# Performance work log

Hardware: AMD Instinct MI355X
Metric: run time of the kernel (lower is better)

The kernel has to match this reference:

```python
import jax, jax.numpy as jnp
import numpy as np

PATCH = 8      # patch_size
NFREQ = 8      # fourie_freq


def _fourier_feats(nH, nW, F, dtype):
    # Per-patch positional Fourier features: sin/cos of normalized patch-center
    # coords at F dyadic frequencies for both axes -> [nH, nW, 4F].
    iy = (jnp.arange(nH, dtype=jnp.float32) + 0.5) / nH
    ix = (jnp.arange(nW, dtype=jnp.float32) + 0.5) / nW
    freqs = (2.0 ** jnp.arange(F, dtype=jnp.float32)) * jnp.pi
    fy = iy[:, None] * freqs[None, :]  # [nH, F]
    fx = ix[:, None] * freqs[None, :]  # [nW, F]
    feats = jnp.concatenate([
        jnp.broadcast_to(jnp.sin(fy)[:, None, :], (nH, nW, F)),
        jnp.broadcast_to(jnp.cos(fy)[:, None, :], (nH, nW, F)),
        jnp.broadcast_to(jnp.sin(fx)[None, :, :], (nH, nW, F)),
        jnp.broadcast_to(jnp.cos(fx)[None, :, :], (nH, nW, F)),
    ], axis=-1)
    return feats.astype(dtype)


def setup_inputs() -> dict:
    key = jax.random.key(0)
    ks = jax.random.split(key, 5)
    B, C, H, W = 16, 64, 128, 128
    E, OC, P, F = 8, 64, PATCH, NFREQ
    GC = C + 4 * F  # gate_channel = 96
    x = jax.random.normal(ks[0], (B, C, H, W), jnp.float32)
    expert_w = jax.random.normal(ks[1], (E, OC, C, 3, 3), jnp.float32) * 0.05
    expert_b = jax.random.normal(ks[2], (E, OC), jnp.float32) * 0.05
    gate_w = jax.random.normal(ks[3], (E, GC * P * P), jnp.float32) * 0.02
    gate_b = jnp.zeros((E,), jnp.float32)
    return {"x": x, "expert_w": expert_w, "expert_b": expert_b,
            "gate_w": gate_w, "gate_b": gate_b}


def reference(x, expert_w, expert_b, gate_w, gate_b):
    B, C, H, W = x.shape
    E, OC = expert_w.shape[0], expert_w.shape[1]
    P, F = PATCH, NFREQ
    nH, nW = H // P, W // P

    # --- gating: per-patch softmax over experts ---
    # patches: [B, nH, nW, C, P, P] (matches nn.Flatten over (C,P,P))
    patches = x.reshape(B, C, nH, P, nW, P).transpose(0, 2, 4, 1, 3, 5)
    feats = _fourier_feats(nH, nW, F, x.dtype)                       # [nH,nW,4F]
    pos = jnp.broadcast_to(feats[None, :, :, :, None, None],
                           (B, nH, nW, 4 * F, P, P))
    gate_in = jnp.concatenate([patches, pos], axis=3).reshape(B, nH, nW, -1)
    logits = jnp.einsum('bhwf,ef->bhwe', gate_in, gate_w) + gate_b
    gate = jax.nn.softmax(logits, axis=-1)                           # [B,nH,nW,E]

    # --- experts: all E convs fused into a single conv, then gated combine ---
    wk = expert_w.reshape(E * OC, C, 3, 3)
    y = jax.lax.conv_general_dilated(
        x, wk, window_strides=(1, 1), padding='SAME',
        dimension_numbers=('NCHW', 'OIHW', 'NCHW'))
    y = y + expert_b.reshape(E * OC)[None, :, None, None]
    y = jax.nn.relu(y).reshape(B, E, OC, H, W)

    # upsample per-patch gates to pixel resolution: [B,E,H,W]
    g = gate.transpose(0, 3, 1, 2)                                   # [B,E,nH,nW]
    g = jnp.repeat(jnp.repeat(g, P, axis=2), P, axis=3)
    out = jnp.einsum('behw,bechw->bchw', g, y)                       # [B,OC,H,W]
    return out
```

## Files before the change

kernel.cpp:

```cpp
#include <hip/hip_runtime.h>

typedef short v8s __attribute__((ext_vector_type(8)));
typedef float v4f __attribute__((ext_vector_type(4)));

#define NCH    64
#define NHH    128
#define NWW    128
#define NOC    64
#define KSTEPS 18

#define CSTR 72
#define COLS 66
#define SLAB_BYTES (6 * COLS * CSTR * 2)
#define BBUF_OFF   SLAB_BYTES
#define LDSG_OFF   (SLAB_BYTES + 16384)
#define SMEM_BYTES 73728

__device__ __forceinline__ unsigned short f2bf(float f) {
  unsigned int u = __float_as_uint(f);
  u += 0x7FFFu + ((u >> 16) & 1u);
  return (unsigned short)(u >> 16);
}

__global__ void pack_b_kernel(const float* __restrict__ ew,
                              unsigned short* __restrict__ bp) {
  int f = blockIdx.x * 256 + threadIdx.x;
  int j = f & 7;
  int t = f >> 3;
  int lane = t & 63;
  t >>= 6;
  int nt = t & 3;
  t >>= 2;
  int s = t % KSTEPS;
  int e = t / KSTEPS;
  int k = s * 32 + (lane >> 4) * 8 + j;
  int n = nt * 16 + (lane & 15);
  int khw = k >> 6;
  int c = k & 63;
  bp[f] = f2bf(ew[((e * NOC + n) * NCH + c) * 9 + khw]);
}

__global__ void gate_kernel(const float* __restrict__ x,
                            const float* __restrict__ gw,
                            const float* __restrict__ gb,
                            float* __restrict__ gate_out) {
  int pid = blockIdx.x;
  int pw = pid & 15;
  int ph = (pid >> 4) & 15;
  int b  = pid >> 8;
  int tid = threadIdx.x;

  float cy = (ph + 0.5f) / 16.0f;
  float cx = (pw + 0.5f) / 16.0f;

  float acc[8];
#pragma unroll
  for (int e = 0; e < 8; ++e) acc[e] = 0.f;

  for (int u = tid; u < 1024; u += 256) {
    int ch = u >> 4;
    int pix = (u & 15) * 4;
    int py = pix >> 3;
    int px = pix & 7;
    const float4 xv = *(const float4*)&x[((b * NCH + ch) * NHH + ph * 8 + py) * NWW + pw * 8 + px];
    int fidx = ch * 64 + pix;
#pragma unroll
    for (int e = 0; e < 8; ++e) {
      const float4 wv = *(const float4*)&gw[e * 6144 + fidx];
      acc[e] += xv.x * wv.x + xv.y * wv.y + xv.z * wv.z + xv.w * wv.w;
    }
  }
  for (int u = tid; u < 512; u += 256) {
    int j = u >> 4;
    int g4 = (u & 15) * 4;
    float freq = (float)(1 << (j & 7)) * 3.14159265358979323846f;
    float base = (j < 16) ? cy : cx;
    float a = base * freq;
    float v = ((j >> 3) & 1) ? cosf(a) : sinf(a);
    int fidx = 4096 + j * 64 + g4;
#pragma unroll
    for (int e = 0; e < 8; ++e) {
      const float4 wv = *(const float4*)&gw[e * 6144 + fidx];
      acc[e] += v * (wv.x + wv.y + wv.z + wv.w);
    }
  }

#pragma unroll
  for (int e = 0; e < 8; ++e)
    for (int off = 32; off > 0; off >>= 1)
      acc[e] += __shfl_down(acc[e], off, 64);

  __shared__ float red[8][4];
  int wid = tid >> 6;
  int lane = tid & 63;
  if (lane == 0) {
#pragma unroll
    for (int e = 0; e < 8; ++e) red[e][wid] = acc[e];
  }
  __syncthreads();
  if (tid == 0) {
    float lg[8];
    float mx = -1e30f;
#pragma unroll
    for (int e = 0; e < 8; ++e) {
      lg[e] = red[e][0] + red[e][1] + red[e][2] + red[e][3] + gb[e];
      mx = fmaxf(mx, lg[e]);
    }
    float sum = 0.f;
#pragma unroll
    for (int e = 0; e < 8; ++e) { lg[e] = expf(lg[e] - mx); sum += lg[e]; }
    float inv = 1.0f / sum;
#pragma unroll
    for (int e = 0; e < 8; ++e) gate_out[pid * 8 + e] = lg[e] * inv;
  }
}

__device__ __forceinline__ void load_stage(const unsigned short* __restrict__ bp,
                                           char* smem, int gs, int buf,
                                           int wid, int lane) {
  const char* gsrc = (const char*)bp + gs * 8192 + wid * 2048 + lane * 16;
  char* ldst = smem + BBUF_OFF + buf * 8192 + wid * 2048;
  __builtin_amdgcn_global_load_lds(
      (const __attribute__((address_space(1))) void*)gsrc,
      (__attribute__((address_space(3))) void*)ldst, 16, 0, 0);
  __builtin_amdgcn_global_load_lds(
      (const __attribute__((address_space(1))) void*)(gsrc + 1024),
      (__attribute__((address_space(3))) void*)(ldst + 1024), 16, 0, 0);
}

__global__ __launch_bounds__(256, 2) void moe_conv_kernel(
    const float* __restrict__ x,
    const float* __restrict__ eb,
    const unsigned short* __restrict__ bp,
    const float* __restrict__ gate,
    float* __restrict__ out) {
  __shared__ __align__(16) char smem[SMEM_BYTES];
  unsigned short* slab = (unsigned short*)smem;
  unsigned short* bbufs = (unsigned short*)(smem + BBUF_OFF);
  float* ldsg = (float*)(smem + LDSG_OFF);

  const int tid = threadIdx.x;
  const int bid = blockIdx.x;
  const int wseg = bid & 1;
  const int hq = (bid >> 1) & 31;
  const int b = bid >> 6;
  const int w0 = wseg * 64;
  const int wid = tid >> 6;
  const int lane = tid & 63;
  const int quad = lane >> 4;
  const int l15 = lane & 15;
  const int rp  = wid >> 1;
  const int och = wid & 1;
  const int ntb = och * 2;

  load_stage(bp, smem, 0, 0, wid, lane);

  if (tid < 64) {
    ldsg[tid] = gate[((b * 16 + (hq >> 1)) * 16 + wseg * 8 + (tid >> 3)) * 8 + (tid & 7)];
  }

  const int hbase = hq * 4 - 1;
  const int wbase = w0 - 1;
  for (int flat = tid; flat < 6 * 32 * COLS; flat += 256) {
    int col = flat % COLS;
    int t = flat / COLS;
    int cp = t & 31;
    int r = t >> 5;
    int gh = hbase + r;
    int gw_ = wbase + col;
    float v0 = 0.f, v1 = 0.f;
    if (((unsigned)gh < 128u) && ((unsigned)gw_ < 128u)) {
      const float* px = x + (((b * NCH + cp * 2) * NHH + gh) * NWW + gw_);
      v0 = px[0];
      v1 = px[NHH * NWW];
    }
    unsigned int pk = (unsigned int)f2bf(v0) | ((unsigned int)f2bf(v1) << 16);
    *(unsigned int*)&slab[(r * COLS + col) * CSTR + cp * 2] = pk;
  }
  __syncthreads();

  const v4f vzero = {0.f, 0.f, 0.f, 0.f};
  v4f oacc[8][2];
#pragma unroll
  for (int mt = 0; mt < 8; ++mt) {
    oacc[mt][0] = vzero;
    oacc[mt][1] = vzero;
  }

  const unsigned short* abase = &slab[(rp * 2 * COLS + l15) * CSTR + quad * 8];

  for (int e = 0; e < 8; ++e) {
    v4f vacc[8][2];
#pragma unroll
    for (int mt = 0; mt < 8; ++mt) {
      vacc[mt][0] = vzero;
      vacc[mt][1] = vzero;
    }

#pragma unroll
    for (int st = 0; st < 9; ++st) {
      const int gs = e * 9 + st;
      if (gs > 0) __syncthreads();
      if (gs + 1 < 72) load_stage(bp, smem, gs + 1, (gs + 1) & 1, wid, lane);

      const unsigned short* bstage = bbufs + (gs & 1) * 4096;
#pragma unroll
      for (int sub = 0; sub < 2; ++sub) {
        const int sl = st * 2 + sub;
        const int kh = sl / 6;
        const int kw = (sl / 2) % 3;
        const int ch = sl & 1;
        const v8s b0 = *(const v8s*)(bstage + (sub * 4 + ntb) * 512 + lane * 8);
        const v8s b1 = *(const v8s*)(bstage + (sub * 4 + ntb + 1) * 512 + lane * 8);
#pragma unroll
        for (int mt = 0; mt < 8; ++mt) {
          const v8s a = *(const v8s*)(abase +
              (((mt >> 2) + kh) * COLS + (mt & 3) * 16 + kw) * CSTR + ch * 32);
          vacc[mt][0] = __builtin_amdgcn_mfma_f32_16x16x32_bf16(a, b0, vacc[mt][0], 0, 0, 0);
          vacc[mt][1] = __builtin_amdgcn_mfma_f32_16x16x32_bf16(a, b1, vacc[mt][1], 0, 0, 0);
        }
      }
    }

    float bias0 = eb[e * NOC + ntb * 16 + l15];
    float bias1 = eb[e * NOC + (ntb + 1) * 16 + l15];
#pragma unroll
    for (int mt = 0; mt < 8; ++mt) {
      float g = ldsg[((mt & 3) * 2 + (quad >> 1)) * 8 + e];
#pragma unroll
      for (int r = 0; r < 4; ++r) {
        float v0 = fmaxf(vacc[mt][0][r] + bias0, 0.f);
        float v1 = fmaxf(vacc[mt][1][r] + bias1, 0.f);
        oacc[mt][0][r] += v0 * g;
        oacc[mt][1][r] += v1 * g;
      }
    }
  }

  __syncthreads();
  float* tb = (float*)smem + wid * 4352;
#pragma unroll
  for (int i = 0; i < 2; ++i)
#pragma unroll
    for (int mt = 0; mt < 8; ++mt)
      *(v4f*)(tb + (mt >> 2) * 2176 + (i * 16 + l15) * 68 + (mt & 3) * 16 + quad * 4) =
          oacc[mt][i];

  const int h0 = hq * 4 + rp * 2;
#pragma unroll
  for (int r2 = 0; r2 < 2; ++r2) {
    const int h = h0 + r2;
#pragma unroll
    for (int g4 = 0; g4 < 8; ++g4) {
      const int ocl = g4 * 4 + quad;
      const v4f vv = *(const v4f*)(tb + r2 * 2176 + ocl * 68 + l15 * 4);
      float* dst = out + ((b * NOC + och * 32 + ocl) * NHH + h) * NWW + w0 + l15 * 4;
      *(v4f*)dst = vv;
    }
  }
}

extern "C" void kernel_launch(void* const* d_in, const int* in_sizes, int n_in,
                              void* d_out, int out_size, void* d_ws, size_t ws_size,
                              hipStream_t stream) {
  const float* x  = (const float*)d_in[0];
  const float* ew = (const float*)d_in[1];
  const float* eb = (const float*)d_in[2];
  const float* gw = (const float*)d_in[3];
  const float* gb = (const float*)d_in[4];
  float* out = (float*)d_out;

  unsigned short* bp = (unsigned short*)d_ws;
  float* gate = (float*)((char*)d_ws + 589824);

  hipLaunchKernelGGL(pack_b_kernel, dim3(1152), dim3(256), 0, stream, ew, bp);
  hipLaunchKernelGGL(gate_kernel, dim3(4096), dim3(256), 0, stream, x, gw, gb, gate);
  hipLaunchKernelGGL(moe_conv_kernel, dim3(1024), dim3(256), 0, stream, x, eb, bp, gate, out);
}
```

Baseline: 303.6 us.

## Process expert pairs per stage to reuse A fragments across two experts

Repacks the expert weight buffer so each 8 KB stage holds one k-step for two experts instead of two k-steps for one expert. Each stage's A fragments are then loaded once from LDS and used for both experts' MFMAs, halving A-fragment LDS reads. In exchange, accumulator registers double (two sets of 64 floats of vacc plus oacc), which risks spilling or lower occupancy under launch_bounds(256,2).

```diff
diff --git a/kernel.cpp b/kernel.cpp
--- a/kernel.cpp
+++ b/kernel.cpp
@@ -31,13 +31,14 @@
   t >>= 6;
   int nt = t & 3;
   t >>= 2;
+  int e2 = t & 1;
+  t >>= 1;
   int s = t % KSTEPS;
-  int e = t / KSTEPS;
+  int ep = t / KSTEPS;
+  int e = ep * 2 + e2;
   int k = s * 32 + (lane >> 4) * 8 + j;
   int n = nt * 16 + (lane & 15);
-  int khw = k >> 6;
-  int c = k & 63;
-  bp[f] = f2bf(ew[((e * NOC + n) * NCH + c) * 9 + khw]);
+  bp[f] = f2bf(ew[((e * NOC + n) * NCH + (k & 63)) * 9 + (k >> 6)]);
 }
 
 __global__ void gate_kernel(const float* __restrict__ x,
@@ -189,50 +190,60 @@
 
   const unsigned short* abase = &slab[(rp * 2 * COLS + l15) * CSTR + quad * 8];
 
-  for (int e = 0; e < 8; ++e) {
-    v4f vacc[8][2];
-#pragma unroll
-    for (int mt = 0; mt < 8; ++mt) {
-      vacc[mt][0] = vzero;
-      vacc[mt][1] = vzero;
-    }
-
-#pragma unroll
-    for (int st = 0; st < 9; ++st) {
-      const int gs = e * 9 + st;
+  for (int ep = 0; ep < 4; ++ep) {
+    v4f vacc[2][8][2];
+#pragma unroll
+    for (int e2 = 0; e2 < 2; ++e2)
+#pragma unroll
+      for (int mt = 0; mt < 8; ++mt) {
+        vacc[e2][mt][0] = vzero;
+        vacc[e2][mt][1] = vzero;
+      }
+
+#pragma unroll
+    for (int s = 0; s < KSTEPS; ++s) {
+      const int gs = ep * KSTEPS + s;
       if (gs > 0) __syncthreads();
       if (gs + 1 < 72) load_stage(bp, smem, gs + 1, (gs + 1) & 1, wid, lane);
 
       const unsigned short* bstage = bbufs + (gs & 1) * 4096;
-#pragma unroll
-      for (int sub = 0; sub < 2; ++sub) {
-        const int sl = st * 2 + sub;
-        const int kh = sl / 6;
-        const int kw = (sl / 2) % 3;
-        const int ch = sl & 1;
-        const v8s b0 = *(const v8s*)(bstage + (sub * 4 + ntb) * 512 + lane * 8);
-        const v8s b1 = *(const v8s*)(bstage + (sub * 4 + ntb + 1) * 512 + lane * 8);
+      const int kh = s / 6;
+      const int kw = (s / 2) % 3;
+      const int ch = s & 1;
+
+      v8s af[8];
+#pragma unroll
+      for (int mt = 0; mt < 8; ++mt)
+        af[mt] = *(const v8s*)(abase +
+            (((mt >> 2) + kh) * COLS + (mt & 3) * 16 + kw) * CSTR + ch * 32);
+
+#pragma unroll
+      for (int e2 = 0; e2 < 2; ++e2) {
+        const v8s b0 = *(const v8s*)(bstage + (e2 * 4 + ntb) * 512 + lane * 8);
+        const v8s b1 = *(const v8s*)(bstage + (e2 * 4 + ntb + 1) * 512 + lane * 8);
 #pragma unroll
         for (int mt = 0; mt < 8; ++mt) {
-          const v8s a = *(const v8s*)(abase +
-              (((mt >> 2) + kh) * COLS + (mt & 3) * 16 + kw) * CSTR + ch * 32);
-          vacc[mt][0] = __builtin_amdgcn_mfma_f32_16x16x32_bf16(a, b0, vacc[mt][0], 0, 0, 0);
-          vacc[mt][1] = __builtin_amdgcn_mfma_f32_16x16x32_bf16(a, b1, vacc[mt][1], 0, 0, 0);
+          vacc[e2][mt][0] = __builtin_amdgcn_mfma_f32_16x16x32_bf16(af[mt], b0, vacc[e2][mt][0], 0, 0, 0);
+          vacc[e2][mt][1] = __builtin_amdgcn_mfma_f32_16x16x32_bf16(af[mt], b1, vacc[e2][mt][1], 0, 0, 0);
         }
       }
     }
 
-    float bias0 = eb[e * NOC + ntb * 16 + l15];
-    float bias1 = eb[e * NOC + (ntb + 1) * 16 + l15];
-#pragma unroll
-    for (int mt = 0; mt < 8; ++mt) {
-      float g = ldsg[((mt & 3) * 2 + (quad >> 1)) * 8 + e];
-#pragma unroll
-      for (int r = 0; r < 4; ++r) {
-        float v0 = fmaxf(vacc[mt][0][r] + bias0, 0.f);
-        float v1 = fmaxf(vacc[mt][1][r] + bias1, 0.f);
-        oacc[mt][0][r] += v0 * g;
-        oacc[mt][1][r] += v1 * g;
+#pragma unroll
+    for (int e2 = 0; e2 < 2; ++e2) {
+      const int e = ep * 2 + e2;
+      float bias0 = eb[e * NOC + ntb * 16 + l15];
+      float bias1 = eb[e * NOC + (ntb + 1) * 16 + l15];
+#pragma unroll
+      for (int mt = 0; mt < 8; ++mt) {
+        float g = ldsg[((mt & 3) * 2 + (quad >> 1)) * 8 + e];
+#pragma unroll
+        for (int r = 0; r < 4; ++r) {
+          float v0 = fmaxf(vacc[e2][mt][0][r] + bias0, 0.f);
+          float v1 = fmaxf(vacc[e2][mt][1][r] + bias1, 0.f);
+          oacc[mt][0][r] += v0 * g;
+          oacc[mt][1][r] += v1 * g;
+        }
       }
     }
   }
```

Result: slower. 309.8 us (+2.0%).

## Replace block-wide B double-buffer with per-wave 3-slot DMA ring

Applied to the files above, without the earlier changes.

Each wave now streams only the weight fragments it needs into a private 3-deep LDS ring, using vmcnt waits instead of a block-wide __syncthreads at every K step. The packed weight layout is reordered so each output-channel half is contiguous per step. Gate values move from LDS into a register that is read with shuffles. This removes 72 barriers per block and lets waves drift independently. The cost is redundant weight loads across the two waves sharing an output half, and correctness now depends on hand-written waitcnt counts.

```diff
diff --git a/kernel.cpp b/kernel.cpp
--- a/kernel.cpp
+++ b/kernel.cpp
@@ -12,9 +12,10 @@
 #define CSTR 72
 #define COLS 66
 #define SLAB_BYTES (6 * COLS * CSTR * 2)
-#define BBUF_OFF   SLAB_BYTES
-#define LDSG_OFF   (SLAB_BYTES + 16384)
-#define SMEM_BYTES 73728
+#define RING_OFF   SLAB_BYTES
+#define RING_SLOTS 3
+#define RING_WAVE_BYTES (RING_SLOTS * 2048)
+#define SMEM_BYTES (SLAB_BYTES + 4 * RING_WAVE_BYTES)
 
 __device__ __forceinline__ unsigned short f2bf(float f) {
   unsigned int u = __float_as_uint(f);
@@ -26,18 +27,16 @@
                               unsigned short* __restrict__ bp) {
   int f = blockIdx.x * 256 + threadIdx.x;
   int j = f & 7;
-  int t = f >> 3;
-  int lane = t & 63;
-  t >>= 6;
-  int nt = t & 3;
-  t >>= 2;
+  int lane = (f >> 3) & 63;
+  int i = (f >> 9) & 1;
+  int och = (f >> 10) & 1;
+  int t = f >> 11;
   int s = t % KSTEPS;
   int e = t / KSTEPS;
+  int nt = och * 2 + i;
   int k = s * 32 + (lane >> 4) * 8 + j;
   int n = nt * 16 + (lane & 15);
-  int khw = k >> 6;
-  int c = k & 63;
-  bp[f] = f2bf(ew[((e * NOC + n) * NCH + c) * 9 + khw]);
+  bp[f] = f2bf(ew[((e * NOC + n) * NCH + (k & 63)) * 9 + (k >> 6)]);
 }
 
 __global__ void gate_kernel(const float* __restrict__ x,
@@ -115,17 +114,10 @@
   }
 }
 
-__device__ __forceinline__ void load_stage(const unsigned short* __restrict__ bp,
-                                           char* smem, int gs, int buf,
-                                           int wid, int lane) {
-  const char* gsrc = (const char*)bp + gs * 8192 + wid * 2048 + lane * 16;
-  char* ldst = smem + BBUF_OFF + buf * 8192 + wid * 2048;
+__device__ __forceinline__ void dma16(const char* gsrc, char* ldst) {
   __builtin_amdgcn_global_load_lds(
       (const __attribute__((address_space(1))) void*)gsrc,
       (__attribute__((address_space(3))) void*)ldst, 16, 0, 0);
-  __builtin_amdgcn_global_load_lds(
-      (const __attribute__((address_space(1))) void*)(gsrc + 1024),
-      (__attribute__((address_space(3))) void*)(ldst + 1024), 16, 0, 0);
 }
 
 __global__ __launch_bounds__(256, 2) void moe_conv_kernel(
@@ -136,8 +128,6 @@
     float* __restrict__ out) {
   __shared__ __align__(16) char smem[SMEM_BYTES];
   unsigned short* slab = (unsigned short*)smem;
-  unsigned short* bbufs = (unsigned short*)(smem + BBUF_OFF);
-  float* ldsg = (float*)(smem + LDSG_OFF);
 
   const int tid = threadIdx.x;
   const int bid = blockIdx.x;
@@ -153,11 +143,9 @@
   const int och = wid & 1;
   const int ntb = och * 2;
 
-  load_stage(bp, smem, 0, 0, wid, lane);
-
-  if (tid < 64) {
-    ldsg[tid] = gate[((b * 16 + (hq >> 1)) * 16 + wseg * 8 + (tid >> 3)) * 8 + (tid & 7)];
-  }
+  char* ringbase = smem + RING_OFF + wid * RING_WAVE_BYTES;
+
+  const float greg = gate[((b * 16 + (hq >> 1)) * 16 + wseg * 8 + (lane >> 3)) * 8 + (lane & 7)];
 
   const int hbase = hq * 4 - 1;
   const int wbase = w0 - 1;
@@ -177,6 +165,15 @@
     unsigned int pk = (unsigned int)f2bf(v0) | ((unsigned int)f2bf(v1) << 16);
     *(unsigned int*)&slab[(r * COLS + col) * CSTR + cp * 2] = pk;
   }
+
+#pragma unroll
+  for (int t = 0; t < 3; ++t) {
+    const char* gsrc = (const char*)bp + t * 4096 + och * 2048 + lane * 16;
+    char* ldst = ringbase + t * 2048;
+    dma16(gsrc, ldst);
+    dma16(gsrc + 1024, ldst + 1024);
+  }
+
   __syncthreads();
 
   const v4f vzero = {0.f, 0.f, 0.f, 0.f};
@@ -190,6 +187,9 @@
   const unsigned short* abase = &slab[(rp * 2 * COLS + l15) * CSTR + quad * 8];
 
   for (int e = 0; e < 8; ++e) {
+    const float bias0 = eb[e * NOC + ntb * 16 + l15];
+    const float bias1 = eb[e * NOC + (ntb + 1) * 16 + l15];
+
     v4f vacc[8][2];
 #pragma unroll
     for (int mt = 0; mt < 8; ++mt) {
@@ -198,35 +198,37 @@
     }
 
 #pragma unroll
-    for (int st = 0; st < 9; ++st) {
-      const int gs = e * 9 + st;
-      if (gs > 0) __syncthreads();
-      if (gs + 1 < 72) load_stage(bp, smem, gs + 1, (gs + 1) & 1, wid, lane);
-
-      const unsigned short* bstage = bbufs + (gs & 1) * 4096;
-#pragma unroll
-      for (int sub = 0; sub < 2; ++sub) {
-        const int sl = st * 2 + sub;
-        const int kh = sl / 6;
-        const int kw = (sl / 2) % 3;
-        const int ch = sl & 1;
-        const v8s b0 = *(const v8s*)(bstage + (sub * 4 + ntb) * 512 + lane * 8);
-        const v8s b1 = *(const v8s*)(bstage + (sub * 4 + ntb + 1) * 512 + lane * 8);
-#pragma unroll
-        for (int mt = 0; mt < 8; ++mt) {
-          const v8s a = *(const v8s*)(abase +
-              (((mt >> 2) + kh) * COLS + (mt & 3) * 16 + kw) * CSTR + ch * 32);
-          vacc[mt][0] = __builtin_amdgcn_mfma_f32_16x16x32_bf16(a, b0, vacc[mt][0], 0, 0, 0);
-          vacc[mt][1] = __builtin_amdgcn_mfma_f32_16x16x32_bf16(a, b1, vacc[mt][1], 0, 0, 0);
-        }
+    for (int s = 0; s < KSTEPS; ++s) {
+      if (s < 3) asm volatile("s_waitcnt vmcnt(6)" ::: "memory");
+      else       asm volatile("s_waitcnt vmcnt(4)" ::: "memory");
+
+      const unsigned short* bslot = (const unsigned short*)(ringbase + (s % 3) * 2048);
+      const v8s b0 = *(const v8s*)(bslot + lane * 8);
+      const v8s b1 = *(const v8s*)(bslot + 512 + lane * 8);
+
+      const int kh = s / 6;
+      const int kw = (s / 2) % 3;
+      const int ch = s & 1;
+#pragma unroll
+      for (int mt = 0; mt < 8; ++mt) {
+        const v8s a = *(const v8s*)(abase +
+            (((mt >> 2) + kh) * COLS + (mt & 3) * 16 + kw) * CSTR + ch * 32);
+        vacc[mt][0] = __builtin_amdgcn_mfma_f32_16x16x32_bf16(a, b0, vacc[mt][0], 0, 0, 0);
+        vacc[mt][1] = __builtin_amdgcn_mfma_f32_16x16x32_bf16(a, b1, vacc[mt][1], 0, 0, 0);
       }
-    }
-
-    float bias0 = eb[e * NOC + ntb * 16 + l15];
-    float bias1 = eb[e * NOC + (ntb + 1) * 16 + l15];
+
+      asm volatile("s_waitcnt lgkmcnt(0)" ::: "memory");
+      int t3 = e * KSTEPS + s + 3;
+      if (t3 > 143) t3 = 143;
+      const char* gsrc = (const char*)bp + t3 * 4096 + och * 2048 + lane * 16;
+      char* ldst = ringbase + (s % 3) * 2048;
+      dma16(gsrc, ldst);
+      dma16(gsrc + 1024, ldst + 1024);
+    }
+
 #pragma unroll
     for (int mt = 0; mt < 8; ++mt) {
-      float g = ldsg[((mt & 3) * 2 + (quad >> 1)) * 8 + e];
+      const float g = __shfl(greg, ((mt & 3) * 2 + (quad >> 1)) * 8 + e, 64);
 #pragma unroll
       for (int r = 0; r < 4; ++r) {
         float v0 = fmaxf(vacc[mt][0][r] + bias0, 0.f);
@@ -237,6 +239,7 @@
     }
   }
 
+  asm volatile("s_waitcnt vmcnt(0)" ::: "memory");
   __syncthreads();
   float* tb = (float*)smem + wid * 4352;
 #pragma unroll
```

New measurement: 307.6 us. Within noise of the previous version (+1.3%).
